# Kernel tuning notes

Hardware: AMD Instinct MI355X
Metric: run time of the kernel (lower is better)

Reference implementation:

```python
import math
import jax, jax.numpy as jnp
import numpy as np

SCALING = 16.0 / 32.0  # alpha / rank


def real_fourier_orthogonal_multiply(c):
    """Vectorized equivalent of the per-frequency Python loop: build a complex
    spectrum from real Fourier coefficients and inverse-rfft along last dim."""
    n = c.shape[-1]
    sqrt_n = math.sqrt(n)
    pair_scale = math.sqrt(n / 2.0)
    max_f = (n - 1) // 2
    work = c.astype(jnp.float32)
    dc = (work[..., 0] * sqrt_n)[..., None].astype(jnp.complex64)
    cos = work[..., 1:1 + 2 * max_f:2] * pair_scale
    sin = work[..., 2:2 + 2 * max_f:2] * pair_scale
    mid = (cos - 1j * sin).astype(jnp.complex64)  # freqs 1..max_f
    parts = [dc, mid]
    if n % 2 == 0:
        parts.append((work[..., -1] * sqrt_n)[..., None].astype(jnp.complex64))
    spectrum = jnp.concatenate(parts, axis=-1)  # [..., n//2+1]
    return jnp.fft.irfft(spectrum, n=n, axis=-1).astype(c.dtype)


def setup_inputs() -> dict:
    key = jax.random.key(0)
    ks = jax.random.split(key, 9)
    B, S, D_in, D_out, R0, R1, E = 4, 2048, 4096, 4096, 32, 8, 3
    x = jax.random.normal(ks[0], (B, S, D_in), dtype=jnp.float32)
    W_base = jax.random.normal(ks[1], (D_out, D_in), dtype=jnp.float32) * 0.02
    b_base = jax.random.normal(ks[2], (D_out,), dtype=jnp.float32) * 0.02
    enc0 = jax.random.normal(ks[3], (R0, D_in), dtype=jnp.float32) * 0.02
    enc1 = jax.random.normal(ks[4], (R1, D_in), dtype=jnp.float32) * 0.02
    coefs0 = jax.random.normal(ks[5], (E, D_out, R0), dtype=jnp.float32) * 0.02
    coefs1 = jax.random.normal(ks[6], (E, D_out, R1), dtype=jnp.float32) * 0.02
    # sparse decoder masks (buffers in the torch module)
    mask0 = jax.random.randint(ks[7], (E, D_out, R0), 0, 2).astype(bool)
    mask1 = jax.random.randint(ks[8], (E, D_out, R1), 0, 2).astype(bool)
    return dict(x=x, W_base=W_base, b_base=b_base, enc0=enc0, enc1=enc1,
                coefs0=coefs0, coefs1=coefs1, mask0=mask0, mask1=mask1)


def reference(x, W_base, b_base, enc0, enc1, coefs0, coefs1, mask0, mask1):
    # base linear
    base = jnp.einsum('bsd,od->bso', x, W_base) + b_base
    # encoder blocks (shared across experts)
    e0 = jnp.einsum('bsd,rd->bsr', x, enc0)  # [B,S,R0]
    e1 = jnp.einsum('bsd,rd->bsr', x, enc1)  # [B,S,R1]
    # masked decoder blocks per expert, summed over blocks
    w0 = coefs0 * mask0.astype(coefs0.dtype)  # [E,O,R0]
    w1 = coefs1 * mask1.astype(coefs1.dtype)  # [E,O,R1]
    decoded = (jnp.einsum('bsr,eor->ebso', e0, w0)
               + jnp.einsum('bsr,eor->ebso', e1, w1))  # [E,B,S,O]
    transformed = real_fourier_orthogonal_multiply(decoded)
    update = transformed.sum(axis=0)  # sum over active experts
    return base + update * SCALING
```

## Files before the change

kernel.cpp:

```cpp
#include <hip/hip_runtime.h>

typedef __attribute__((ext_vector_type(2))) float f32x2;
typedef __attribute__((ext_vector_type(4))) float f32x4;
typedef __attribute__((ext_vector_type(16))) float f32x16;
typedef __attribute__((ext_vector_type(8))) short bf16x8;
typedef __attribute__((ext_vector_type(8))) unsigned short u16x8;

#define GL2LDS(g, l) __builtin_amdgcn_global_load_lds( \
    (const __attribute__((address_space(1))) void*)(g), \
    (__attribute__((address_space(3))) void*)(l), 16, 0, 0)

__device__ __forceinline__ unsigned short f2bf(float x) {
    union { float f; unsigned u; } v; v.f = x;
    unsigned r = (v.u + 0x7FFF + ((v.u >> 16) & 1)) >> 16;
    return (unsigned short)r;
}

__global__ __launch_bounds__(256) void k_prep(const float* __restrict__ c0,
                                              const float* __restrict__ c1,
                                              const int* __restrict__ m0,
                                              const int* __restrict__ m1,
                                              float* __restrict__ Wc,
                                              const float* __restrict__ x,
                                              unsigned short* __restrict__ xb) {
    int b = blockIdx.x;
    if (b < 640) {
        int idx = b * 256 + threadIdx.x;
        if (idx >= 4096 * 40) return;
        int o = idx / 40, c = idx % 40;
        float s = 0.f;
        if (c < 32) {
            #pragma unroll
            for (int e = 0; e < 3; ++e) {
                int i = (e * 4096 + o) * 32 + c;
                s += c0[i] * (m0[i] != 0 ? 1.f : 0.f);
            }
        } else {
            int r = c - 32;
            #pragma unroll
            for (int e = 0; e < 3; ++e) {
                int i = (e * 4096 + o) * 8 + r;
                s += c1[i] * (m1[i] != 0 ? 1.f : 0.f);
            }
        }
        Wc[idx] = s;
    } else {
        int idx = (b - 640) * 256 + threadIdx.x;
        f32x4 f0 = ((const f32x4*)x)[(size_t)idx * 2];
        f32x4 f1 = ((const f32x4*)x)[(size_t)idx * 2 + 1];
        u16x8 o;
        o[0] = f2bf(f0[0]); o[1] = f2bf(f0[1]); o[2] = f2bf(f0[2]); o[3] = f2bf(f0[3]);
        o[4] = f2bf(f1[0]); o[5] = f2bf(f1[1]); o[6] = f2bf(f1[2]); o[7] = f2bf(f1[3]);
        *(u16x8*)(xb + (size_t)idx * 8) = o;
    }
}

__global__ __launch_bounds__(256) void k_gmat(const float* __restrict__ Wc,
                                              float* __restrict__ G) {
    __shared__ float lds[10752];
    int tid = threadIdx.x;
    int t_base = blockIdx.x * 8;
    int f_slot = tid & 31;
    int tg = (tid >> 5) & 1;
    int rg = tid >> 6;
    float acc[4][10];
    #pragma unroll
    for (int a = 0; a < 4; ++a)
        #pragma unroll
        for (int b = 0; b < 10; ++b) acc[a][b] = 0.f;

    for (int ch = 0; ch < 16; ++ch) {
        __syncthreads();
        #pragma unroll
        for (int j = 0; j < 10; ++j) {
            int idx = tid + j * 256;
            int row = idx / 20;
            int v = idx % 20;
            int f = ch * 128 + row;
            f32x4 val = {0.f, 0.f, 0.f, 0.f};
            if (f >= 1) val = *(const f32x4*)(Wc + (2 * f - 1) * 40 + v * 4);
            *(f32x4*)(lds + row * 84 + v * 4) = val;
        }
        __syncthreads();
        #pragma unroll
        for (int j2 = 0; j2 < 4; ++j2) {
            int f_local = f_slot + 32 * j2;
            int f = ch * 128 + f_local;
            float cs[4], sn[4];
            #pragma unroll
            for (int tt = 0; tt < 4; ++tt) {
                int t = t_base + tg * 4 + tt;
                int ph = (f * t) & 4095;
                float rev = (float)ph * (1.0f / 4096.0f);
                cs[tt] = __builtin_amdgcn_cosf(rev);
                sn[tt] = __builtin_amdgcn_sinf(rev);
            }
            const float* Lc = lds + f_local * 84 + rg * 10;
            const float* Ls = Lc + 40;
            #pragma unroll
            for (int rr = 0; rr < 10; ++rr) {
                float wc = Lc[rr], ws = Ls[rr];
                #pragma unroll
                for (int tt = 0; tt < 4; ++tt)
                    acc[tt][rr] += cs[tt] * wc + sn[tt] * ws;
            }
        }
    }
    __syncthreads();
    #pragma unroll
    for (int tt = 0; tt < 4; ++tt)
        #pragma unroll
        for (int rr = 0; rr < 10; ++rr)
            lds[tid * 40 + tt * 10 + rr] = acc[tt][rr];
    __syncthreads();
    for (int oi = tid; oi < 320; oi += 256) {
        int t_local = oi / 40, rc = oi % 40;
        int tg2 = t_local >> 2, tsub = t_local & 3;
        int rg2 = rc / 10, rsub = rc % 10;
        float s = 0.f;
        #pragma unroll
        for (int fs = 0; fs < 32; ++fs)
            s += lds[(fs + tg2 * 32 + rg2 * 64) * 40 + tsub * 10 + rsub];
        int t = t_base + t_local;
        float dc = Wc[rc];
        float ny = Wc[4095 * 40 + rc];
        float sign = (t & 1) ? -1.f : 1.f;
        float g = 0.5f * (0.0220970869120796f * s + (dc + sign * ny) * (1.0f / 64.0f));
        G[t * 40 + rc] = g;
    }
}

__global__ __launch_bounds__(256) void k_wcomb(const float* __restrict__ Wb,
                                               const float* __restrict__ enc0,
                                               const float* __restrict__ enc1,
                                               const float* __restrict__ G,
                                               unsigned short* __restrict__ Wcb) {
    __shared__ float ldsE[40 * 256];
    __shared__ float ldsG[32 * 40];
    int tid = threadIdx.x;
    int d0 = blockIdx.x * 256;
    int t0 = blockIdx.y * 32;
    #pragma unroll
    for (int j = 0; j < 10; ++j) {
        int idx = tid + j * 256;
        int k = idx / 64, v = idx % 64;
        const float* src = (k < 32) ? (enc0 + (size_t)k * 4096) : (enc1 + (size_t)(k - 32) * 4096);
        *(f32x4*)(ldsE + k * 256 + v * 4) = *(const f32x4*)(src + d0 + v * 4);
    }
    #pragma unroll
    for (int j = 0; j < 5; ++j) {
        int idx = tid + j * 256;
        ldsG[idx] = G[(size_t)(t0 + idx / 40) * 40 + (idx % 40)];
    }
    __syncthreads();
    int dg = tid & 31, tg = tid >> 5;
    f32x2 a[4][4];
    #pragma unroll
    for (int s = 0; s < 4; ++s)
        #pragma unroll
        for (int tt = 0; tt < 4; ++tt) a[s][tt] = (f32x2){0.f, 0.f};
    #pragma unroll 8
    for (int r = 0; r < 40; ++r) {
        f32x2 e[4];
        #pragma unroll
        for (int s = 0; s < 4; ++s)
            e[s] = *(const f32x2*)(ldsE + r * 256 + s * 64 + dg * 2);
        #pragma unroll
        for (int tt = 0; tt < 4; ++tt) {
            float g = ldsG[(tg * 4 + tt) * 40 + r];
            #pragma unroll
            for (int s = 0; s < 4; ++s)
                a[s][tt] += g * e[s];
        }
    }
    #pragma unroll
    for (int tt = 0; tt < 4; ++tt) {
        int t = t0 + tg * 4 + tt;
        #pragma unroll
        for (int s = 0; s < 4; ++s) {
            int d = d0 + s * 64 + dg * 2;
            f32x2 wv = *(const f32x2*)(Wb + (size_t)t * 4096 + d);
            f32x2 rv = a[s][tt] + wv;
            unsigned short lo = f2bf(rv[0]), hi = f2bf(rv[1]);
            *(unsigned*)(Wcb + (size_t)t * 4096 + d) = (unsigned)lo | ((unsigned)hi << 16);
        }
    }
}

__global__ __launch_bounds__(512, 2) void k_gemm(const unsigned short* __restrict__ A,
                                                 const unsigned short* __restrict__ B,
                                                 const float* __restrict__ bias,
                                                 float* __restrict__ C) {
    __shared__ __align__(16) short As[2][256 * 64];
    __shared__ __align__(16) short Bs[2][256 * 64];
    const int tid = threadIdx.x;
    const int lane = tid & 63, w = tid >> 6;
    const int wm = w >> 2, wn = w & 3;
    const int col = lane & 31, hi = lane >> 5;
    const int sw = col & 7;

    int bid = blockIdx.x;
    int swz = (bid & 7) * 64 + (bid >> 3);
    int m0 = (swz >> 4) * 256;
    int n0 = (swz & 15) * 256;

    const int srow = w * 8 + (lane >> 3);
    const int scg  = (lane & 7) ^ ((lane >> 3) & 7);
    const unsigned short* Ag = A + (size_t)(m0 + srow) * 4096 + scg * 8;
    const unsigned short* Bg = B + (size_t)(n0 + srow) * 4096 + scg * 8;

#define STAGE(buf, kt) do { \
    _Pragma("unroll") \
    for (int c = 0; c < 4; ++c) { \
        GL2LDS(Ag + (size_t)(c * 64) * 4096 + (kt), &As[buf][(c * 64 + w * 8) * 64]); \
        GL2LDS(Bg + (size_t)(c * 64) * 4096 + (kt), &Bs[buf][(c * 64 + w * 8) * 64]); \
    } \
} while (0)

    int aoff[4], boff[2], co[4];
    #pragma unroll
    for (int mf = 0; mf < 4; ++mf) aoff[mf] = (wm * 128 + mf * 32 + col) * 64;
    #pragma unroll
    for (int nf = 0; nf < 2; ++nf) boff[nf] = (wn * 64 + nf * 32 + col) * 64;
    #pragma unroll
    for (int ks = 0; ks < 4; ++ks) co[ks] = ((ks * 2 + hi) ^ sw) * 8;

    f32x16 acc[4][2];
    #pragma unroll
    for (int mf = 0; mf < 4; ++mf)
        #pragma unroll
        for (int nf = 0; nf < 2; ++nf)
            #pragma unroll
            for (int r = 0; r < 16; ++r) acc[mf][nf][r] = 0.f;

    STAGE(0, 0);
    STAGE(1, 64);
    asm volatile("s_waitcnt vmcnt(8)\n\ts_barrier" ::: "memory");

    for (int t = 0; t < 64; ++t) {
        const int cur = t & 1;
        bf16x8 aLo[2][4], b0[4];
        #pragma unroll
        for (int ks = 0; ks < 4; ++ks) {
            aLo[0][ks] = *(const bf16x8*)&As[cur][aoff[0] + co[ks]];
            aLo[1][ks] = *(const bf16x8*)&As[cur][aoff[1] + co[ks]];
            b0[ks]     = *(const bf16x8*)&Bs[cur][boff[0] + co[ks]];
        }
        asm volatile("s_barrier" ::: "memory");
        __builtin_amdgcn_s_setprio(1);
        #pragma unroll
        for (int ks = 0; ks < 4; ++ks) {
            acc[0][0] = __builtin_amdgcn_mfma_f32_32x32x16_bf16(aLo[0][ks], b0[ks], acc[0][0], 0, 0, 0);
            acc[1][0] = __builtin_amdgcn_mfma_f32_32x32x16_bf16(aLo[1][ks], b0[ks], acc[1][0], 0, 0, 0);
        }
        __builtin_amdgcn_s_setprio(0);
        asm volatile("s_barrier" ::: "memory");
        bf16x8 aHi[2][4];
        #pragma unroll
        for (int ks = 0; ks < 4; ++ks) {
            aHi[0][ks] = *(const bf16x8*)&As[cur][aoff[2] + co[ks]];
            aHi[1][ks] = *(const bf16x8*)&As[cur][aoff[3] + co[ks]];
        }
        asm volatile("s_barrier" ::: "memory");
        __builtin_amdgcn_s_setprio(1);
        #pragma unroll
        for (int ks = 0; ks < 4; ++ks) {
            acc[2][0] = __builtin_amdgcn_mfma_f32_32x32x16_bf16(aHi[0][ks], b0[ks], acc[2][0], 0, 0, 0);
            acc[3][0] = __builtin_amdgcn_mfma_f32_32x32x16_bf16(aHi[1][ks], b0[ks], acc[3][0], 0, 0, 0);
        }
        __builtin_amdgcn_s_setprio(0);
        asm volatile("s_barrier" ::: "memory");
        bf16x8 b1[4];
        #pragma unroll
        for (int ks = 0; ks < 4; ++ks)
            b1[ks] = *(const bf16x8*)&Bs[cur][boff[1] + co[ks]];
        asm volatile("s_barrier" ::: "memory");
        __builtin_amdgcn_s_setprio(1);
        #pragma unroll
        for (int ks = 0; ks < 4; ++ks) {
            acc[2][1] = __builtin_amdgcn_mfma_f32_32x32x16_bf16(aHi[0][ks], b1[ks], acc[2][1], 0, 0, 0);
            acc[3][1] = __builtin_amdgcn_mfma_f32_32x32x16_bf16(aHi[1][ks], b1[ks], acc[3][1], 0, 0, 0);
        }
        __builtin_amdgcn_s_setprio(0);
        asm volatile("s_barrier" ::: "memory");
        if (t + 2 < 64) STAGE(cur, (t + 2) * 64);
        asm volatile("s_barrier" ::: "memory");
        __builtin_amdgcn_s_setprio(1);
        #pragma unroll
        for (int ks = 0; ks < 4; ++ks) {
            acc[0][1] = __builtin_amdgcn_mfma_f32_32x32x16_bf16(aLo[0][ks], b1[ks], acc[0][1], 0, 0, 0);
            acc[1][1] = __builtin_amdgcn_mfma_f32_32x32x16_bf16(aLo[1][ks], b1[ks], acc[1][1], 0, 0, 0);
        }
        __builtin_amdgcn_s_setprio(0);
        if (t + 2 < 64) {
            asm volatile("s_waitcnt vmcnt(8)\n\ts_barrier" ::: "memory");
        } else if (t + 1 < 64) {
            asm volatile("s_waitcnt vmcnt(0)\n\ts_barrier" ::: "memory");
        } else {
            asm volatile("s_barrier" ::: "memory");
        }
    }
#undef STAGE

    #pragma unroll
    for (int nf = 0; nf < 2; ++nf) {
        float bv = bias[n0 + wn * 64 + nf * 32 + col];
        #pragma unroll
        for (int mf = 0; mf < 4; ++mf) {
            #pragma unroll
            for (int r = 0; r < 16; ++r) {
                int row = m0 + wm * 128 + mf * 32 + (r & 3) + 8 * (r >> 2) + 4 * hi;
                C[(size_t)row * 4096 + n0 + wn * 64 + nf * 32 + col] = acc[mf][nf][r] + bv;
            }
        }
    }
}

extern "C" void kernel_launch(void* const* d_in, const int* in_sizes, int n_in,
                              void* d_out, int out_size, void* d_ws, size_t ws_size,
                              hipStream_t stream) {
    const float* x   = (const float*)d_in[0];
    const float* Wb  = (const float*)d_in[1];
    const float* bb  = (const float*)d_in[2];
    const float* e0  = (const float*)d_in[3];
    const float* e1  = (const float*)d_in[4];
    const float* c0  = (const float*)d_in[5];
    const float* c1  = (const float*)d_in[6];
    const int*   m0  = (const int*)d_in[7];
    const int*   m1  = (const int*)d_in[8];
    float* out = (float*)d_out;

    char* ws = (char*)d_ws;
    unsigned short* xb  = (unsigned short*)ws;
    float* Wc           = (float*)(ws + 67108864);
    float* G            = (float*)(ws + 67764224);
    unsigned short* Wcb = (unsigned short*)(ws + 68419584);

    k_prep <<<17024, 256, 0, stream>>>(c0, c1, m0, m1, Wc, x, xb);
    k_gmat <<<512, 256, 0, stream>>>(Wc, G);
    k_wcomb<<<dim3(16, 128), 256, 0, stream>>>(Wb, e0, e1, G, Wcb);
    k_gemm <<<512, 512, 0, stream>>>(xb, Wcb, bb, out);
}
```

Before: 686.9 us.

## Restructure GEMM main loop to one-ahead prefetch with fewer barriers

Replaces the two-stage prefetch loop, which had many intra-iteration barriers, with a manually unrolled pair of tile bodies. Each body issues the next tile's global-to-LDS loads right after the first MFMA group and ends with a single vmcnt(0) plus barrier. The aim is to cut barrier and synchronisation overhead between waves. In exchange the prefetch distance drops from two tiles to one, so load latency may be less hidden.

```diff
diff --git a/kernel.cpp b/kernel.cpp
--- a/kernel.cpp
+++ b/kernel.cpp
@@ -233,73 +233,61 @@
             #pragma unroll
             for (int r = 0; r < 16; ++r) acc[mf][nf][r] = 0.f;
 
+#define TILE_BODY(CB, NB, kt, DO_STAGE) do { \
+    bf16x8 aLo[2][4], aHi[2][4], b0[4], b1[4]; \
+    _Pragma("unroll") \
+    for (int ks = 0; ks < 4; ++ks) { \
+        aLo[0][ks] = *(const bf16x8*)&As[CB][aoff[0] + co[ks]]; \
+        aLo[1][ks] = *(const bf16x8*)&As[CB][aoff[1] + co[ks]]; \
+        b0[ks]     = *(const bf16x8*)&Bs[CB][boff[0] + co[ks]]; \
+    } \
+    __builtin_amdgcn_s_setprio(1); \
+    _Pragma("unroll") \
+    for (int ks = 0; ks < 4; ++ks) { \
+        acc[0][0] = __builtin_amdgcn_mfma_f32_32x32x16_bf16(aLo[0][ks], b0[ks], acc[0][0], 0, 0, 0); \
+        acc[1][0] = __builtin_amdgcn_mfma_f32_32x32x16_bf16(aLo[1][ks], b0[ks], acc[1][0], 0, 0, 0); \
+    } \
+    __builtin_amdgcn_s_setprio(0); \
+    if (DO_STAGE) STAGE(NB, (kt) + 64); \
+    _Pragma("unroll") \
+    for (int ks = 0; ks < 4; ++ks) { \
+        aHi[0][ks] = *(const bf16x8*)&As[CB][aoff[2] + co[ks]]; \
+        aHi[1][ks] = *(const bf16x8*)&As[CB][aoff[3] + co[ks]]; \
+    } \
+    __builtin_amdgcn_s_setprio(1); \
+    _Pragma("unroll") \
+    for (int ks = 0; ks < 4; ++ks) { \
+        acc[2][0] = __builtin_amdgcn_mfma_f32_32x32x16_bf16(aHi[0][ks], b0[ks], acc[2][0], 0, 0, 0); \
+        acc[3][0] = __builtin_amdgcn_mfma_f32_32x32x16_bf16(aHi[1][ks], b0[ks], acc[3][0], 0, 0, 0); \
+    } \
+    __builtin_amdgcn_s_setprio(0); \
+    _Pragma("unroll") \
+    for (int ks = 0; ks < 4; ++ks) \
+        b1[ks] = *(const bf16x8*)&Bs[CB][boff[1] + co[ks]]; \
+    __builtin_amdgcn_s_setprio(1); \
+    _Pragma("unroll") \
+    for (int ks = 0; ks < 4; ++ks) { \
+        acc[2][1] = __builtin_amdgcn_mfma_f32_32x32x16_bf16(aHi[0][ks], b1[ks], acc[2][1], 0, 0, 0); \
+        acc[3][1] = __builtin_amdgcn_mfma_f32_32x32x16_bf16(aHi[1][ks], b1[ks], acc[3][1], 0, 0, 0); \
+    } \
+    _Pragma("unroll") \
+    for (int ks = 0; ks < 4; ++ks) { \
+        acc[0][1] = __builtin_amdgcn_mfma_f32_32x32x16_bf16(aLo[0][ks], b1[ks], acc[0][1], 0, 0, 0); \
+        acc[1][1] = __builtin_amdgcn_mfma_f32_32x32x16_bf16(aLo[1][ks], b1[ks], acc[1][1], 0, 0, 0); \
+    } \
+    __builtin_amdgcn_s_setprio(0); \
+    asm volatile("s_waitcnt vmcnt(0)\n\ts_barrier" ::: "memory"); \
+} while (0)
+
     STAGE(0, 0);
-    STAGE(1, 64);
-    asm volatile("s_waitcnt vmcnt(8)\n\ts_barrier" ::: "memory");
-
-    for (int t = 0; t < 64; ++t) {
-        const int cur = t & 1;
-        bf16x8 aLo[2][4], b0[4];
-        #pragma unroll
-        for (int ks = 0; ks < 4; ++ks) {
-            aLo[0][ks] = *(const bf16x8*)&As[cur][aoff[0] + co[ks]];
-            aLo[1][ks] = *(const bf16x8*)&As[cur][aoff[1] + co[ks]];
-            b0[ks]     = *(const bf16x8*)&Bs[cur][boff[0] + co[ks]];
-        }
-        asm volatile("s_barrier" ::: "memory");
-        __builtin_amdgcn_s_setprio(1);
-        #pragma unroll
-        for (int ks = 0; ks < 4; ++ks) {
-            acc[0][0] = __builtin_amdgcn_mfma_f32_32x32x16_bf16(aLo[0][ks], b0[ks], acc[0][0], 0, 0, 0);
-            acc[1][0] = __builtin_amdgcn_mfma_f32_32x32x16_bf16(aLo[1][ks], b0[ks], acc[1][0], 0, 0, 0);
-        }
-        __builtin_amdgcn_s_setprio(0);
-        asm volatile("s_barrier" ::: "memory");
-        bf16x8 aHi[2][4];
-        #pragma unroll
-        for (int ks = 0; ks < 4; ++ks) {
-            aHi[0][ks] = *(const bf16x8*)&As[cur][aoff[2] + co[ks]];
-            aHi[1][ks] = *(const bf16x8*)&As[cur][aoff[3] + co[ks]];
-        }
-        asm volatile("s_barrier" ::: "memory");
-        __builtin_amdgcn_s_setprio(1);
-        #pragma unroll
-        for (int ks = 0; ks < 4; ++ks) {
-            acc[2][0] = __builtin_amdgcn_mfma_f32_32x32x16_bf16(aHi[0][ks], b0[ks], acc[2][0], 0, 0, 0);
-            acc[3][0] = __builtin_amdgcn_mfma_f32_32x32x16_bf16(aHi[1][ks], b0[ks], acc[3][0], 0, 0, 0);
-        }
-        __builtin_amdgcn_s_setprio(0);
-        asm volatile("s_barrier" ::: "memory");
-        bf16x8 b1[4];
-        #pragma unroll
-        for (int ks = 0; ks < 4; ++ks)
-            b1[ks] = *(const bf16x8*)&Bs[cur][boff[1] + co[ks]];
-        asm volatile("s_barrier" ::: "memory");
-        __builtin_amdgcn_s_setprio(1);
-        #pragma unroll
-        for (int ks = 0; ks < 4; ++ks) {
-            acc[2][1] = __builtin_amdgcn_mfma_f32_32x32x16_bf16(aHi[0][ks], b1[ks], acc[2][1], 0, 0, 0);
-            acc[3][1] = __builtin_amdgcn_mfma_f32_32x32x16_bf16(aHi[1][ks], b1[ks], acc[3][1], 0, 0, 0);
-        }
-        __builtin_amdgcn_s_setprio(0);
-        asm volatile("s_barrier" ::: "memory");
-        if (t + 2 < 64) STAGE(cur, (t + 2) * 64);
-        asm volatile("s_barrier" ::: "memory");
-        __builtin_amdgcn_s_setprio(1);
-        #pragma unroll
-        for (int ks = 0; ks < 4; ++ks) {
-            acc[0][1] = __builtin_amdgcn_mfma_f32_32x32x16_bf16(aLo[0][ks], b1[ks], acc[0][1], 0, 0, 0);
-            acc[1][1] = __builtin_amdgcn_mfma_f32_32x32x16_bf16(aLo[1][ks], b1[ks], acc[1][1], 0, 0, 0);
-        }
-        __builtin_amdgcn_s_setprio(0);
-        if (t + 2 < 64) {
-            asm volatile("s_waitcnt vmcnt(8)\n\ts_barrier" ::: "memory");
-        } else if (t + 1 < 64) {
-            asm volatile("s_waitcnt vmcnt(0)\n\ts_barrier" ::: "memory");
-        } else {
-            asm volatile("s_barrier" ::: "memory");
-        }
-    }
+    asm volatile("s_waitcnt vmcnt(0)\n\ts_barrier" ::: "memory");
+
+    for (int i = 0; i < 32; ++i) {
+        int kt = i * 128;
+        TILE_BODY(0, 1, kt, true);
+        TILE_BODY(1, 0, kt + 64, (i < 31));
+    }
+#undef TILE_BODY
 #undef STAGE
 
     #pragma unroll
```

New measurement: 625.1 us. 9.0% less time.
